# Kernel optimization log

Measured on AMD Instinct MI355X. Metric: run time of the kernel, lower is better.

Reference implementation:

```python
import jax, jax.numpy as jnp
import numpy as np

E = 192; Q = 48; H = 3; HD = Q // H  # per-branch embed 48, 3 heads of 16
CONV_CH = 4; K = 15; PAD = K // 2


def layer_norm(x, g, b, eps=1e-6):
    m = jnp.mean(x, axis=-1, keepdims=True)
    v = jnp.mean((x - m) ** 2, axis=-1, keepdims=True)
    return (x - m) * jax.lax.rsqrt(v + eps) * g + b


def mha(x, w_in, b_in, w_o, b_o):
    # x: [B,S,48]; torch nn.MultiheadAttention math (dropout=eval/identity)
    B, S, _ = x.shape
    qkv = x @ w_in.T + b_in                      # [B,S,144]
    q, k, v = jnp.split(qkv, 3, axis=-1)
    q = q.reshape(B, S, H, HD)
    k = k.reshape(B, S, H, HD)
    v = v.reshape(B, S, H, HD)
    scores = jnp.einsum('bqhd,bkhd->bhqk', q, k) / jnp.sqrt(jnp.float32(HD))
    attn = jax.nn.softmax(scores, axis=-1)
    out = jnp.einsum('bhqk,bkhd->bqhd', attn, v).reshape(B, S, Q)
    return out @ w_o.T + b_o


def light_conv(x96, conv_w):
    # x96: [B,S,96] -> view(-1, 4, 96), depthwise conv1d (k=15, pad=7), view back
    B, S, W = x96.shape
    r = x96.reshape(-1, CONV_CH, W)              # [B*S/... wait: B*S*96/(4*96)=B*S/4? No: reshape(-1,4,96) => [B*S, ...]
    y = jax.lax.conv_general_dilated(
        r, conv_w, window_strides=(1,), padding=[(PAD, PAD)],
        dimension_numbers=('NCH', 'OIH', 'NCH'), feature_group_count=CONV_CH)
    return y.reshape(B, S, W)


def setup_inputs() -> dict:
    key = jax.random.key(0)
    ks = jax.random.split(key, 16)
    sc = 0.05
    d = {
        'x': jax.random.normal(ks[0], (128, 512, E), dtype=jnp.float32),
        'ln1_g': jnp.ones((E,), jnp.float32), 'ln1_b': jnp.zeros((E,), jnp.float32),
        'acc_wqkv': jax.random.normal(ks[1], (3 * Q, Q), jnp.float32) * sc,
        'acc_bqkv': jnp.zeros((3 * Q,), jnp.float32),
        'acc_wo': jax.random.normal(ks[2], (Q, Q), jnp.float32) * sc,
        'acc_bo': jnp.zeros((Q,), jnp.float32),
        'gyro_wqkv': jax.random.normal(ks[3], (3 * Q, Q), jnp.float32) * sc,
        'gyro_bqkv': jnp.zeros((3 * Q,), jnp.float32),
        'gyro_wo': jax.random.normal(ks[4], (Q, Q), jnp.float32) * sc,
        'gyro_bo': jnp.zeros((Q,), jnp.float32),
        'conv_w': jax.random.normal(ks[5], (CONV_CH, 1, K), jnp.float32) * sc,
        'ln2_g': jnp.ones((E,), jnp.float32), 'ln2_b': jnp.zeros((E,), jnp.float32),
        'w1': jax.random.normal(ks[6], (2 * E, E), jnp.float32) * sc,
        'b1': jnp.zeros((2 * E,), jnp.float32),
        'w2': jax.random.normal(ks[7], (E, 2 * E), jnp.float32) * sc,
        'b2': jnp.zeros((E,), jnp.float32),
    }
    return d


def reference(x, ln1_g, ln1_b, acc_wqkv, acc_bqkv, acc_wo, acc_bo,
              gyro_wqkv, gyro_bqkv, gyro_wo, gyro_bo, conv_w,
              ln2_g, ln2_b, w1, b1, w2, b2):
    xn = layer_norm(x, ln1_g, ln1_b)
    x_conv = light_conv(xn[:, :, 48:144], conv_w)
    x_acc = mha(xn[:, :, 0:48], acc_wqkv, acc_bqkv, acc_wo, acc_bo)
    x_gyro = mha(xn[:, :, 96:144], gyro_wqkv, gyro_bqkv, gyro_wo, gyro_bo)
    xcat = jnp.concatenate([x_acc, x_conv, x_gyro], axis=2)
    x1 = xcat + x
    tt = layer_norm(x1, ln2_g, ln2_b)
    tt = jax.nn.relu(tt @ w1.T + b1)
    tt = jax.nn.relu(tt @ w2.T + b2)
    return x1 + tt
```

## Files before the change

kernel.cpp:

```cpp
#include <hip/hip_runtime.h>
#include <stdint.h>

typedef unsigned short u16;
typedef short bf16x8 __attribute__((ext_vector_type(8)));
typedef float f32x4 __attribute__((ext_vector_type(4)));
typedef float f32x16 __attribute__((ext_vector_type(16)));
typedef uint32_t u32x4 __attribute__((ext_vector_type(4)));

#define NB   128
#define SEQ  512
#define EMB  192
#define NTOK (NB * SEQ)
#define F1DIM 384
#define ATTW 128
#define VTP  520
#define KTS  24
#define XnS  200
#define X1S  196
#define H1S  392

__device__ __forceinline__ float bf2f(u16 u) {
  union { uint32_t u; float f; } v; v.u = ((uint32_t)u) << 16; return v.f;
}
__device__ __forceinline__ u16 f2bf(float f) {
  union { float f; uint32_t u; } v; v.f = f;
  uint32_t r = v.u + 0x7fffu + ((v.u >> 16) & 1u);
  return (u16)(r >> 16);
}
__device__ __forceinline__ uint32_t pack2bf(float a, float b) {
  return (uint32_t)f2bf(a) | ((uint32_t)f2bf(b) << 16);
}

__global__ __launch_bounds__(256) void pack_kernel(const float* __restrict__ w1,
    const float* __restrict__ w2, const float* __restrict__ wqa,
    const float* __restrict__ wqg, const float* __restrict__ woa,
    const float* __restrict__ wog, u16* __restrict__ w1b, u16* __restrict__ w2b,
    u16* __restrict__ wqp, u16* __restrict__ wop) {
  int idx = (int)blockIdx.x * 256 + (int)threadIdx.x;
  if (idx < 73728) {
    w1b[idx] = f2bf(w1[idx]);
  } else if (idx < 147456) {
    w2b[idx - 73728] = f2bf(w2[idx - 73728]);
  } else if (idx < 165888) {
    int i = idx - 147456;
    int row = i >> 6, k = i & 63;
    float v = 0.0f;
    if (k < 48) v = (row < 144) ? wqa[row * 48 + k] : wqg[(row - 144) * 48 + k];
    wqp[i] = f2bf(v);
  } else if (idx < 172032) {
    int i = idx - 165888;
    int row = i >> 6, k = i & 63;
    float v = 0.0f;
    if (k < 48) v = (row < 48) ? woa[row * 48 + k] : wog[(row - 48) * 48 + k];
    wop[i] = f2bf(v);
  }
}

__global__ __launch_bounds__(256) void ln1_qkv_conv_kernel(
    const float* __restrict__ x, const float* __restrict__ g,
    const float* __restrict__ b, const u16* __restrict__ wq,
    const float* __restrict__ bacc, const float* __restrict__ bgyr,
    const float* __restrict__ cw, u16* __restrict__ qkv,
    float* __restrict__ out) {
  __shared__ u16 Xn[64 * XnS];
  int bm = (int)blockIdx.x * 64;
  int tid = threadIdx.x;
  int trow = tid >> 2, part = tid & 3;
  int tok = bm + trow;
  const float* xr = x + (size_t)tok * EMB + part * 48;
  float vals[48];
#pragma unroll
  for (int j = 0; j < 48; j += 4) {
    float4 v = *(const float4*)(xr + j);
    vals[j] = v.x; vals[j + 1] = v.y; vals[j + 2] = v.z; vals[j + 3] = v.w;
  }
  float s = 0.0f, s2 = 0.0f;
#pragma unroll
  for (int j = 0; j < 48; j++) { s += vals[j]; s2 += vals[j] * vals[j]; }
  s += __shfl_xor(s, 1); s2 += __shfl_xor(s2, 1);
  s += __shfl_xor(s, 2); s2 += __shfl_xor(s2, 2);
  float mean = s * (1.0f / EMB);
  float var  = s2 * (1.0f / EMB) - mean * mean;
  float rs   = rsqrtf(var + 1e-6f);
  {
    u16* xnrow = Xn + trow * XnS + part * 48;
    const float* gp = g + part * 48;
    const float* bp = b + part * 48;
#pragma unroll
    for (int j = 0; j < 48; j += 2) {
      uint32_t w = pack2bf((vals[j] - mean) * rs * gp[j] + bp[j],
                           (vals[j + 1] - mean) * rs * gp[j + 1] + bp[j + 1]);
      *(uint32_t*)(xnrow + j) = w;
    }
  }
  __syncthreads();
  int wid = tid >> 6, lane = tid & 63;
  int l15 = lane & 15, quad = lane >> 4;
  const u16* arow_l = Xn + (wid * 16 + l15) * XnS;
  f32x4 acc[18] = {};
#pragma unroll
  for (int ks = 0; ks < 2; ks++) {
    int kk = ks * 32;
    bf16x8 af_a = *(const bf16x8*)(arow_l + kk + quad * 8);
    bf16x8 af_g = *(const bf16x8*)(arow_l + 96 + kk + quad * 8);
#pragma unroll
    for (int st = 0; st < 18; st++) {
      bf16x8 bf = *(const bf16x8*)(wq + (size_t)(st * 16 + l15) * 64 + kk + quad * 8);
      acc[st] = __builtin_amdgcn_mfma_f32_16x16x32_bf16(st < 9 ? af_a : af_g,
                                                        bf, acc[st], 0, 0, 0);
    }
  }
#pragma unroll
  for (int st = 0; st < 18; st++) {
    int col = st * 16 + l15;
    int cc = (col < 144) ? col : col - 144;
    float bias = (col < 144) ? bacc[cc] : bgyr[cc];
    float qs = (cc < 48) ? 0.36067376022f : 1.0f;
#pragma unroll
    for (int r = 0; r < 4; r++) {
      int orow = bm + wid * 16 + quad * 4 + r;
      qkv[(size_t)orow * 288 + col] = f2bf((acc[st][r] + bias) * qs);
    }
  }
  {
    int wr = trow & 3;
    float w15[15];
#pragma unroll
    for (int k = 0; k < 15; k++) w15[k] = cw[wr * 15 + k];
    float win[38];
    int base = part * 24 - 7;
#pragma unroll
    for (int i = 0; i < 38; i++) {
      int p = base + i;
      win[i] = (p >= 0 && p < 96) ? bf2f(Xn[trow * XnS + 48 + p]) : 0.0f;
    }
    const float* xres = x + (size_t)tok * EMB + 48 + part * 24;
    float* orow = out + (size_t)tok * EMB + 48 + part * 24;
#pragma unroll
    for (int c = 0; c < 24; c += 4) {
      float4 r4 = *(const float4*)(xres + c);
      float o[4];
#pragma unroll
      for (int u = 0; u < 4; u++) {
        float sc = 0.0f;
#pragma unroll
        for (int k = 0; k < 15; k++) sc += win[c + u + k] * w15[k];
        o[u] = sc;
      }
      float4 st4 = { o[0] + r4.x, o[1] + r4.y, o[2] + r4.z, o[3] + r4.w };
      *(float4*)(orow + c) = st4;
    }
  }
}

__global__ __launch_bounds__(256) void attn_kernel(const u16* __restrict__ qkv,
                                                   u16* __restrict__ att) {
  __shared__ u16 Kt[SEQ * KTS];
  __shared__ u16 Vt[17 * VTP];
  int bid = blockIdx.x;
  int hh  = bid % 3;
  int brb = (bid / 3) & 1;
  int b   = bid / 6;
  int tid = threadIdx.x;
  size_t tokbase = (size_t)b * SEQ;
  int qoff = brb * 144 + hh * 16;
  int koff = qoff + 48;
  int voff = qoff + 96;
  for (int r = tid; r < SEQ; r += 256) {
    const u16* src = qkv + (tokbase + r) * 288;
    *(uint4*)(Kt + r * KTS)     = *(const uint4*)(src + koff);
    *(uint4*)(Kt + r * KTS + 8) = *(const uint4*)(src + koff + 8);
    u16 tmp[16];
    *(uint4*)(tmp)     = *(const uint4*)(src + voff);
    *(uint4*)(tmp + 8) = *(const uint4*)(src + voff + 8);
#pragma unroll
    for (int j = 0; j < 16; j++) Vt[j * VTP + r] = tmp[j];
  }
  Vt[16 * VTP + tid]       = 0x3F80;
  Vt[16 * VTP + 256 + tid] = 0x3F80;
  __syncthreads();
  int wave = tid >> 6, lane = tid & 63;
  int q31 = lane & 31, h = lane >> 5;
  int dcl = (q31 < 16) ? q31 : 16;
#pragma unroll 1
  for (int qi = 0; qi < 4; qi++) {
    int qrow = (wave * 4 + qi) * 32 + q31;
    bf16x8 qfrag = *(const bf16x8*)(qkv + (tokbase + qrow) * 288 + qoff + h * 8);
    f32x16 Ot = {};
#pragma unroll 2
    for (int kt = 0; kt < 16; kt++) {
      bf16x8 kfrag = *(const bf16x8*)(Kt + (kt * 32 + q31) * KTS + h * 8);
      f32x16 zc = {};
      f32x16 S = __builtin_amdgcn_mfma_f32_32x32x16_bf16(kfrag, qfrag, zc, 0, 0, 0);
      uint32_t pk[8], swk[8];
#pragma unroll
      for (int i = 0; i < 8; i++) {
        union { float f; uint32_t u; } a0, a1;
        a0.f = exp2f(S[2 * i]);
        a1.f = exp2f(S[2 * i + 1]);
        pk[i] = __builtin_amdgcn_perm(a1.u, a0.u, 0x07060302u);
        swk[i] = (uint32_t)__shfl_xor((int)pk[i], 32);
      }
      u32x4 t1 = { h ? swk[2] : pk[0], h ? swk[3] : pk[1],
                   h ? pk[2]  : swk[0], h ? pk[3]  : swk[1] };
      u32x4 t2 = { h ? swk[6] : pk[4], h ? swk[7] : pk[5],
                   h ? pk[6]  : swk[4], h ? pk[7]  : swk[5] };
      bf16x8 pb1 = __builtin_bit_cast(bf16x8, t1);
      bf16x8 pb2 = __builtin_bit_cast(bf16x8, t2);
      bf16x8 av1 = *(const bf16x8*)(Vt + dcl * VTP + kt * 32 + h * 8);
      bf16x8 av2 = *(const bf16x8*)(Vt + dcl * VTP + kt * 32 + 16 + h * 8);
      Ot = __builtin_amdgcn_mfma_f32_32x32x16_bf16(av1, pb1, Ot, 0, 0, 0);
      Ot = __builtin_amdgcn_mfma_f32_32x32x16_bf16(av2, pb2, Ot, 0, 0, 0);
    }
    float inv = 1.0f / Ot[8];
    u16* orow = att + (tokbase + qrow) * ATTW + brb * 48 + hh * 16 + 4 * h;
    uint2 st0 = { pack2bf(Ot[0] * inv, Ot[1] * inv),
                  pack2bf(Ot[2] * inv, Ot[3] * inv) };
    uint2 st1 = { pack2bf(Ot[4] * inv, Ot[5] * inv),
                  pack2bf(Ot[6] * inv, Ot[7] * inv) };
    *(uint2*)(orow)     = st0;
    *(uint2*)(orow + 8) = st1;
  }
}

__global__ __launch_bounds__(512) void tail_kernel(
    const u16* __restrict__ att, const u16* __restrict__ wo,
    const float* __restrict__ boacc, const float* __restrict__ bogyr,
    const float* __restrict__ x, const float* __restrict__ g2,
    const float* __restrict__ b2v, const u16* __restrict__ w1b,
    const float* __restrict__ b1, const u16* __restrict__ w2b,
    const float* __restrict__ b2, float* __restrict__ out) {
  __shared__ float X1[64 * X1S];
  __shared__ u16 Tn[64 * XnS];
  u16* H1 = (u16*)X1;
  int bm = (int)blockIdx.x * 64;
  int tid = threadIdx.x;
  int wid = tid >> 6, lane = tid & 63;
  int l15 = lane & 15, quad = lane >> 4;
  if (tid < 256) {
    int trow = tid >> 2, part = tid & 3;
    const float* src = out + (size_t)(bm + trow) * EMB + 48 + part * 24;
    float* dst = X1 + trow * X1S + 48 + part * 24;
#pragma unroll
    for (int c = 0; c < 24; c += 4) *(float4*)(dst + c) = *(const float4*)(src + c);
  }
  {
    int mt = wid & 3, ng = wid >> 2;
    int row = bm + mt * 16 + l15;
    const u16* arow = att + (size_t)row * ATTW + (ng ? 48 : 0);
    f32x4 acc[3] = {};
#pragma unroll
    for (int ks = 0; ks < 2; ks++) {
      int kk = ks * 32;
      bf16x8 af = *(const bf16x8*)(arow + kk + quad * 8);
#pragma unroll
      for (int st = 0; st < 3; st++) {
        int stg = ng * 3 + st;
        bf16x8 bf = *(const bf16x8*)(wo + (size_t)(stg * 16 + l15) * 64 + kk + quad * 8);
        acc[st] = __builtin_amdgcn_mfma_f32_16x16x32_bf16(af, bf, acc[st], 0, 0, 0);
      }
    }
#pragma unroll
    for (int st = 0; st < 3; st++) {
      int col = (ng * 3 + st) * 16 + l15;
      float bias = (col < 48) ? boacc[col] : bogyr[col - 48];
      int oc = (col < 48) ? col : col + 96;
#pragma unroll
      for (int r = 0; r < 4; r++) {
        int lrow = mt * 16 + quad * 4 + r;
        size_t oi = (size_t)(bm + lrow) * EMB + oc;
        float v = acc[st][r] + bias + x[oi];
        out[oi] = v;
        X1[lrow * X1S + oc] = v;
      }
    }
  }
  __syncthreads();
  {
    int trow = tid >> 3, part = tid & 7;
    const float* xl = X1 + trow * X1S + part * 24;
    float vals[24];
#pragma unroll
    for (int j = 0; j < 24; j += 4) {
      float4 v = *(const float4*)(xl + j);
      vals[j] = v.x; vals[j + 1] = v.y; vals[j + 2] = v.z; vals[j + 3] = v.w;
    }
    float s = 0.0f, s2 = 0.0f;
#pragma unroll
    for (int j = 0; j < 24; j++) { s += vals[j]; s2 += vals[j] * vals[j]; }
    s += __shfl_xor(s, 1); s2 += __shfl_xor(s2, 1);
    s += __shfl_xor(s, 2); s2 += __shfl_xor(s2, 2);
    s += __shfl_xor(s, 4); s2 += __shfl_xor(s2, 4);
    float mean = s * (1.0f / EMB);
    float var  = s2 * (1.0f / EMB) - mean * mean;
    float rs   = rsqrtf(var + 1e-6f);
    u16* trp = Tn + trow * XnS + part * 24;
    const float* gp = g2 + part * 24;
    const float* bp = b2v + part * 24;
#pragma unroll
    for (int j = 0; j < 24; j += 2) {
      uint32_t w = pack2bf((vals[j] - mean) * rs * gp[j] + bp[j],
                           (vals[j + 1] - mean) * rs * gp[j + 1] + bp[j + 1]);
      *(uint32_t*)(trp + j) = w;
    }
  }
  __syncthreads();
  {
    int mg = wid & 1, ng = wid >> 1;
    f32x4 acc1[12] = {};
#pragma unroll
    for (int kk = 0; kk < 192; kk += 32) {
      bf16x8 a0 = *(const bf16x8*)(Tn + (mg * 32 + l15) * XnS + kk + quad * 8);
      bf16x8 a1 = *(const bf16x8*)(Tn + (mg * 32 + 16 + l15) * XnS + kk + quad * 8);
#pragma unroll
      for (int stl = 0; stl < 6; stl++) {
        bf16x8 bf = *(const bf16x8*)(w1b + (size_t)((ng * 6 + stl) * 16 + l15) * EMB + kk + quad * 8);
        acc1[stl]     = __builtin_amdgcn_mfma_f32_16x16x32_bf16(a0, bf, acc1[stl], 0, 0, 0);
        acc1[6 + stl] = __builtin_amdgcn_mfma_f32_16x16x32_bf16(a1, bf, acc1[6 + stl], 0, 0, 0);
      }
    }
    __syncthreads();
#pragma unroll
    for (int stl = 0; stl < 6; stl++) {
      int col = (ng * 6 + stl) * 16 + l15;
      float bias = b1[col];
#pragma unroll
      for (int m2 = 0; m2 < 2; m2++) {
#pragma unroll
        for (int r = 0; r < 4; r++) {
          float v = acc1[m2 * 6 + stl][r] + bias;
          v = v > 0.0f ? v : 0.0f;
          H1[(mg * 32 + m2 * 16 + quad * 4 + r) * H1S + col] = f2bf(v);
        }
      }
    }
  }
  __syncthreads();
  {
    int mg2 = wid & 1, ng2 = wid >> 1;
    f32x4 acc2[6] = {};
#pragma unroll
    for (int kk = 0; kk < 384; kk += 32) {
      bf16x8 a0 = *(const bf16x8*)(H1 + (mg2 * 32 + l15) * H1S + kk + quad * 8);
      bf16x8 a1 = *(const bf16x8*)(H1 + (mg2 * 32 + 16 + l15) * H1S + kk + quad * 8);
#pragma unroll
      for (int stl = 0; stl < 3; stl++) {
        bf16x8 bf = *(const bf16x8*)(w2b + (size_t)((ng2 * 3 + stl) * 16 + l15) * F1DIM + kk + quad * 8);
        acc2[stl]     = __builtin_amdgcn_mfma_f32_16x16x32_bf16(a0, bf, acc2[stl], 0, 0, 0);
        acc2[3 + stl] = __builtin_amdgcn_mfma_f32_16x16x32_bf16(a1, bf, acc2[3 + stl], 0, 0, 0);
      }
    }
#pragma unroll
    for (int stl = 0; stl < 3; stl++) {
      int col = (ng2 * 3 + stl) * 16 + l15;
      float bias = b2[col];
#pragma unroll
      for (int m2 = 0; m2 < 2; m2++) {
#pragma unroll
        for (int r = 0; r < 4; r++) {
          size_t oi = (size_t)(bm + mg2 * 32 + m2 * 16 + quad * 4 + r) * EMB + col;
          float v = acc2[m2 * 3 + stl][r] + bias;
          v = v > 0.0f ? v : 0.0f;
          out[oi] = out[oi] + v;
        }
      }
    }
  }
}

extern "C" void kernel_launch(void* const* d_in, const int* in_sizes, int n_in,
                              void* d_out, int out_size, void* d_ws, size_t ws_size,
                              hipStream_t stream) {
  const float* x         = (const float*)d_in[0];
  const float* ln1_g     = (const float*)d_in[1];
  const float* ln1_b     = (const float*)d_in[2];
  const float* acc_wqkv  = (const float*)d_in[3];
  const float* acc_bqkv  = (const float*)d_in[4];
  const float* acc_wo    = (const float*)d_in[5];
  const float* acc_bo    = (const float*)d_in[6];
  const float* gyro_wqkv = (const float*)d_in[7];
  const float* gyro_bqkv = (const float*)d_in[8];
  const float* gyro_wo   = (const float*)d_in[9];
  const float* gyro_bo   = (const float*)d_in[10];
  const float* conv_w    = (const float*)d_in[11];
  const float* ln2_g     = (const float*)d_in[12];
  const float* ln2_b     = (const float*)d_in[13];
  const float* w1        = (const float*)d_in[14];
  const float* b1        = (const float*)d_in[15];
  const float* w2        = (const float*)d_in[16];
  const float* b2        = (const float*)d_in[17];
  float* out = (float*)d_out;
  char* ws = (char*)d_ws;

  u16* qkvb = (u16*)(ws);
  u16* attb = (u16*)(ws + 37748736);
  u16* w1b  = (u16*)(ws + 54525952);
  u16* w2b  = (u16*)(ws + 54673408);
  u16* wqp  = (u16*)(ws + 54820864);
  u16* wop  = (u16*)(ws + 54857728);

  pack_kernel<<<672, 256, 0, stream>>>(w1, w2, acc_wqkv, gyro_wqkv, acc_wo,
                                       gyro_wo, w1b, w2b, wqp, wop);
  ln1_qkv_conv_kernel<<<NTOK / 64, 256, 0, stream>>>(
      x, ln1_g, ln1_b, wqp, acc_bqkv, gyro_bqkv, conv_w, qkvb, out);
  attn_kernel<<<NB * 6, 256, 0, stream>>>(qkvb, attb);
  tail_kernel<<<NTOK / 64, 512, 0, stream>>>(
      attb, wop, acc_bo, gyro_bo, x, ln2_g, ln2_b, w1b, b1, w2b, b2, out);
}
```

Before: 327.4 us.

## Store conv residual as bf16 in att buffer and keep x1 in bf16 LDS

The conv branch output (plus residual) is now written as bf16 into a widened attention buffer instead of as fp32 into the output tensor. The tail kernel reads it from there and keeps x1 in bf16 shared memory, then writes the final output once instead of doing a read-modify-write on out. This cuts global traffic: no fp32 intermediate write and reread, and no out load in the epilogue. It also lowers LDS use. The cost is precision: the x1 residual is now rounded to bf16 before being added to the final output.

```diff
diff --git a/kernel.cpp b/kernel.cpp
--- a/kernel.cpp
+++ b/kernel.cpp
@@ -12,11 +12,10 @@
 #define EMB  192
 #define NTOK (NB * SEQ)
 #define F1DIM 384
-#define ATTW 128
+#define ATTW 192
 #define VTP  520
 #define KTS  24
 #define XnS  200
-#define X1S  196
 #define H1S  392
 
 __device__ __forceinline__ float bf2f(u16 u) {
@@ -61,7 +60,7 @@
     const float* __restrict__ b, const u16* __restrict__ wq,
     const float* __restrict__ bacc, const float* __restrict__ bgyr,
     const float* __restrict__ cw, u16* __restrict__ qkv,
-    float* __restrict__ out) {
+    u16* __restrict__ att) {
   __shared__ u16 Xn[64 * XnS];
   int bm = (int)blockIdx.x * 64;
   int tid = threadIdx.x;
@@ -135,7 +134,7 @@
       win[i] = (p >= 0 && p < 96) ? bf2f(Xn[trow * XnS + 48 + p]) : 0.0f;
     }
     const float* xres = x + (size_t)tok * EMB + 48 + part * 24;
-    float* orow = out + (size_t)tok * EMB + 48 + part * 24;
+    u16* orow = att + (size_t)tok * ATTW + 96 + part * 24;
 #pragma unroll
     for (int c = 0; c < 24; c += 4) {
       float4 r4 = *(const float4*)(xres + c);
@@ -147,8 +146,8 @@
         for (int k = 0; k < 15; k++) sc += win[c + u + k] * w15[k];
         o[u] = sc;
       }
-      float4 st4 = { o[0] + r4.x, o[1] + r4.y, o[2] + r4.z, o[3] + r4.w };
-      *(float4*)(orow + c) = st4;
+      *(uint32_t*)(orow + c)     = pack2bf(o[0] + r4.x, o[1] + r4.y);
+      *(uint32_t*)(orow + c + 2) = pack2bf(o[2] + r4.z, o[3] + r4.w);
     }
   }
 }
@@ -230,19 +229,21 @@
     const float* __restrict__ b2v, const u16* __restrict__ w1b,
     const float* __restrict__ b1, const u16* __restrict__ w2b,
     const float* __restrict__ b2, float* __restrict__ out) {
-  __shared__ float X1[64 * X1S];
-  __shared__ u16 Tn[64 * XnS];
-  u16* H1 = (u16*)X1;
+  __shared__ u16 LDSB[64 * XnS + 64 * H1S];
+  u16* X1b = LDSB;
+  u16* Tn  = LDSB + 64 * XnS;
+  u16* H1  = LDSB + 64 * XnS;
   int bm = (int)blockIdx.x * 64;
   int tid = threadIdx.x;
   int wid = tid >> 6, lane = tid & 63;
   int l15 = lane & 15, quad = lane >> 4;
-  if (tid < 256) {
-    int trow = tid >> 2, part = tid & 3;
-    const float* src = out + (size_t)(bm + trow) * EMB + 48 + part * 24;
-    float* dst = X1 + trow * X1S + 48 + part * 24;
-#pragma unroll
-    for (int c = 0; c < 24; c += 4) *(float4*)(dst + c) = *(const float4*)(src + c);
+  {
+    int trow = tid >> 3, p8 = tid & 7;
+    const u16* src = att + (size_t)(bm + trow) * ATTW + 96 + p8 * 12;
+    u16* dst = X1b + trow * XnS + 48 + p8 * 12;
+    *(uint2*)(dst)     = *(const uint2*)(src);
+    *(uint2*)(dst + 4) = *(const uint2*)(src + 4);
+    *(uint2*)(dst + 8) = *(const uint2*)(src + 8);
   }
   {
     int mt = wid & 3, ng = wid >> 2;
@@ -268,22 +269,23 @@
 #pragma unroll
       for (int r = 0; r < 4; r++) {
         int lrow = mt * 16 + quad * 4 + r;
-        size_t oi = (size_t)(bm + lrow) * EMB + oc;
-        float v = acc[st][r] + bias + x[oi];
-        out[oi] = v;
-        X1[lrow * X1S + oc] = v;
+        float v = acc[st][r] + bias + x[(size_t)(bm + lrow) * EMB + oc];
+        X1b[lrow * XnS + oc] = f2bf(v);
       }
     }
   }
   __syncthreads();
   {
     int trow = tid >> 3, part = tid & 7;
-    const float* xl = X1 + trow * X1S + part * 24;
+    const u16* xl = X1b + trow * XnS + part * 24;
     float vals[24];
-#pragma unroll
-    for (int j = 0; j < 24; j += 4) {
-      float4 v = *(const float4*)(xl + j);
-      vals[j] = v.x; vals[j + 1] = v.y; vals[j + 2] = v.z; vals[j + 3] = v.w;
+    {
+      u16 raw[24];
+      *(uint4*)(raw)      = *(const uint4*)(xl);
+      *(uint4*)(raw + 8)  = *(const uint4*)(xl + 8);
+      *(uint4*)(raw + 16) = *(const uint4*)(xl + 16);
+#pragma unroll
+      for (int j = 0; j < 24; j++) vals[j] = bf2f(raw[j]);
     }
     float s = 0.0f, s2 = 0.0f;
 #pragma unroll
@@ -305,33 +307,31 @@
     }
   }
   __syncthreads();
-  {
-    int mg = wid & 1, ng = wid >> 1;
-    f32x4 acc1[12] = {};
-#pragma unroll
-    for (int kk = 0; kk < 192; kk += 32) {
-      bf16x8 a0 = *(const bf16x8*)(Tn + (mg * 32 + l15) * XnS + kk + quad * 8);
-      bf16x8 a1 = *(const bf16x8*)(Tn + (mg * 32 + 16 + l15) * XnS + kk + quad * 8);
-#pragma unroll
-      for (int stl = 0; stl < 6; stl++) {
-        bf16x8 bf = *(const bf16x8*)(w1b + (size_t)((ng * 6 + stl) * 16 + l15) * EMB + kk + quad * 8);
-        acc1[stl]     = __builtin_amdgcn_mfma_f32_16x16x32_bf16(a0, bf, acc1[stl], 0, 0, 0);
-        acc1[6 + stl] = __builtin_amdgcn_mfma_f32_16x16x32_bf16(a1, bf, acc1[6 + stl], 0, 0, 0);
-      }
-    }
-    __syncthreads();
+  int mg = wid & 1, ng = wid >> 1;
+  f32x4 acc1[12] = {};
+#pragma unroll
+  for (int kk = 0; kk < 192; kk += 32) {
+    bf16x8 a0 = *(const bf16x8*)(Tn + (mg * 32 + l15) * XnS + kk + quad * 8);
+    bf16x8 a1 = *(const bf16x8*)(Tn + (mg * 32 + 16 + l15) * XnS + kk + quad * 8);
 #pragma unroll
     for (int stl = 0; stl < 6; stl++) {
-      int col = (ng * 6 + stl) * 16 + l15;
-      float bias = b1[col];
-#pragma unroll
-      for (int m2 = 0; m2 < 2; m2++) {
-#pragma unroll
-        for (int r = 0; r < 4; r++) {
-          float v = acc1[m2 * 6 + stl][r] + bias;
-          v = v > 0.0f ? v : 0.0f;
-          H1[(mg * 32 + m2 * 16 + quad * 4 + r) * H1S + col] = f2bf(v);
-        }
+      bf16x8 bf = *(const bf16x8*)(w1b + (size_t)((ng * 6 + stl) * 16 + l15) * EMB + kk + quad * 8);
+      acc1[stl]     = __builtin_amdgcn_mfma_f32_16x16x32_bf16(a0, bf, acc1[stl], 0, 0, 0);
+      acc1[6 + stl] = __builtin_amdgcn_mfma_f32_16x16x32_bf16(a1, bf, acc1[6 + stl], 0, 0, 0);
+    }
+  }
+  __syncthreads();
+#pragma unroll
+  for (int stl = 0; stl < 6; stl++) {
+    int col = (ng * 6 + stl) * 16 + l15;
+    float bias = b1[col];
+#pragma unroll
+    for (int m2 = 0; m2 < 2; m2++) {
+#pragma unroll
+      for (int r = 0; r < 4; r++) {
+        float v = acc1[m2 * 6 + stl][r] + bias;
+        v = v > 0.0f ? v : 0.0f;
+        H1[(mg * 32 + m2 * 16 + quad * 4 + r) * H1S + col] = f2bf(v);
       }
     }
   }
@@ -358,10 +358,10 @@
       for (int m2 = 0; m2 < 2; m2++) {
 #pragma unroll
         for (int r = 0; r < 4; r++) {
-          size_t oi = (size_t)(bm + mg2 * 32 + m2 * 16 + quad * 4 + r) * EMB + col;
+          int lrow = mg2 * 32 + m2 * 16 + quad * 4 + r;
           float v = acc2[m2 * 3 + stl][r] + bias;
           v = v > 0.0f ? v : 0.0f;
-          out[oi] = out[oi] + v;
+          out[(size_t)(bm + lrow) * EMB + col] = v + bf2f(X1b[lrow * XnS + col]);
         }
       }
     }
@@ -394,15 +394,15 @@
 
   u16* qkvb = (u16*)(ws);
   u16* attb = (u16*)(ws + 37748736);
-  u16* w1b  = (u16*)(ws + 54525952);
-  u16* w2b  = (u16*)(ws + 54673408);
-  u16* wqp  = (u16*)(ws + 54820864);
-  u16* wop  = (u16*)(ws + 54857728);
+  u16* w1b  = (u16*)(ws + 62914560);
+  u16* w2b  = (u16*)(ws + 63062016);
+  u16* wqp  = (u16*)(ws + 63209472);
+  u16* wop  = (u16*)(ws + 63246336);
 
   pack_kernel<<<672, 256, 0, stream>>>(w1, w2, acc_wqkv, gyro_wqkv, acc_wo,
                                        gyro_wo, w1b, w2b, wqp, wop);
   ln1_qkv_conv_kernel<<<NTOK / 64, 256, 0, stream>>>(
-      x, ln1_g, ln1_b, wqp, acc_bqkv, gyro_bqkv, conv_w, qkvb, out);
+      x, ln1_g, ln1_b, wqp, acc_bqkv, gyro_bqkv, conv_w, qkvb, attb);
   attn_kernel<<<NB * 6, 256, 0, stream>>>(qkvb, attb);
   tail_kernel<<<NTOK / 64, 512, 0, stream>>>(
       attb, wop, acc_bo, gyro_bo, x, ln2_g, ln2_b, w1b, b1, w2b, b2, out);
```

New measurement: 307.7 us. 6.0% less time.
